# Optimization experiments

Hardware: AMD Instinct MI355X
Metric: run time of the kernel (lower is better)

## Reference

```python
import jax, jax.numpy as jnp
import numpy as np

B, S, D, H, DFF, L = 4, 1024, 512, 8, 2048, 4
HD = D // H


def _make_masks(key):
    k1, k2, k3 = jax.random.split(key, 3)
    node = jax.random.randint(k1, (B, S), 0, 128)            # entity-row id per token
    table = node % 4                                          # table id consistent per node
    col = jax.random.randint(k2, (B, S), 0, 32)               # column-name id
    f2p = jax.random.randint(k3, (B, S, 8), 0, 128)           # fk->pk neighbor node ids
    f2p = f2p.at[:, :, 0].set(node)                           # include self so diag is valid
    active = jnp.ones((B, S, S), dtype=bool)                  # no padding
    same_node = node[:, :, None] == node[:, None, :]
    kv_in_f2p = (node[:, None, :, None] == f2p[:, :, None, :]).any(-1)
    q_in_p2f = (node[:, :, None, None] == f2p[:, None, :, :]).any(-1)
    same_col_table = (col[:, :, None] == col[:, None, :]) & (table[:, :, None] == table[:, None, :])
    col_mask = same_col_table & active
    feat_mask = (same_node | kv_in_f2p) & active
    nbr_mask = q_in_p2f & active
    return col_mask, feat_mask, nbr_mask, active


def setup_inputs() -> dict:
    key = jax.random.key(0)
    ks = jax.random.split(key, 8)
    x = jax.random.normal(ks[0], (B, S, D), dtype=jnp.float32)
    norm_w = jnp.ones((L, 5, D), dtype=jnp.float32)
    attn_w = jax.random.normal(ks[1], (L, 4, 4, D, D), dtype=jnp.float32) * (D ** -0.5)
    ffn_up = jax.random.normal(ks[2], (L, D, DFF), dtype=jnp.float32) * (D ** -0.5)
    ffn_gate = jax.random.normal(ks[3], (L, D, DFF), dtype=jnp.float32) * (D ** -0.5)
    ffn_down = jax.random.normal(ks[4], (L, DFF, D), dtype=jnp.float32) * (DFF ** -0.5)
    col_mask, feat_mask, nbr_mask, full_mask = _make_masks(ks[5])
    return {"x": x, "norm_w": norm_w, "attn_w": attn_w, "ffn_up": ffn_up,
            "ffn_gate": ffn_gate, "ffn_down": ffn_down, "col_mask": col_mask,
            "feat_mask": feat_mask, "nbr_mask": nbr_mask, "full_mask": full_mask}


def _rmsnorm(x, w):
    eps = jnp.finfo(x.dtype).eps
    return x * jax.lax.rsqrt(jnp.mean(x * x, axis=-1, keepdims=True) + eps) * w


def _masked_attn(x, mask, w):
    # w: [4, D, D] = (wq, wk, wv, wo); mask: [b, s, s] bool
    b, s, d = x.shape
    def split_heads(y):
        return y.reshape(b, s, H, HD).transpose(0, 2, 1, 3)  # b h s hd
    q = split_heads(x @ w[0])
    k = split_heads(x @ w[1])
    v = split_heads(x @ w[2])
    scores = jnp.einsum('bhqd,bhkd->bhqk', q, k) * (HD ** -0.5)
    m = mask[:, None, :, :]
    neg = jnp.where(m, scores, -1e30)
    mx = jnp.max(neg, axis=-1, keepdims=True)
    e = jnp.exp(neg - mx) * m
    den = jnp.maximum(e.sum(axis=-1, keepdims=True), 1e-20)  # fully-masked rows -> 0 output
    out = jnp.einsum('bhqk,bhkd->bhqd', e / den, v)
    out = out.transpose(0, 2, 1, 3).reshape(b, s, d)
    return out @ w[3]


def _ffn(x, up, gate, down):
    return (jax.nn.silu(x @ gate) * (x @ up)) @ down


def reference(x, norm_w, attn_w, ffn_up, ffn_gate, ffn_down, col_mask, feat_mask, nbr_mask, full_mask):
    masks = (col_mask, feat_mask, nbr_mask, full_mask)

    def block(h, p):
        nw, aw, up, gate, down = p
        for i in range(4):
            h = h + _masked_attn(_rmsnorm(h, nw[i]), masks[i], aw[i])
        h = h + _ffn(_rmsnorm(h, nw[4]), up, gate, down)
        return h, None

    out, _ = jax.lax.scan(block, x, (norm_w, attn_w, ffn_up, ffn_gate, ffn_down))
    return out
```

## Files before the change

### kernel.cpp

```cpp
#include <hip/hip_runtime.h>
#include <cstdint>
#include <cstddef>

#define B_   4
#define S_   1024
#define D_   512
#define H_   8
#define HD_  64
#define DFF_ 2048
#define L_   4
#define M_   (B_ * S_)

typedef unsigned long long ull;
typedef __attribute__((ext_vector_type(8))) short bf16x8;
typedef __attribute__((ext_vector_type(4))) float f32x4;

__device__ __forceinline__ ushort f2bf(float f) {
  uint32_t u = __float_as_uint(f);
  u += 0x7fffu + ((u >> 16) & 1u);
  return (ushort)(u >> 16);
}
__device__ __forceinline__ float bf2f(ushort b) {
  return __uint_as_float(((uint32_t)b) << 16);
}
__device__ __forceinline__ void g2lds16(const void* g, void* l) {
  __builtin_amdgcn_global_load_lds((const __attribute__((address_space(1))) unsigned int*)g,
                                   (__attribute__((address_space(3))) unsigned int*)l, 16, 0, 0);
}

__global__ __launch_bounds__(256) void wtrans_kernel(const float* __restrict__ in,
                                                     ushort* __restrict__ out,
                                                     int R, int C, size_t ims, size_t oms) {
  __shared__ float tile[32][33];
  const int tx = threadIdx.x & 31, ty = threadIdx.x >> 5;
  const int c0 = blockIdx.x * 32, r0 = blockIdx.y * 32;
  const float* ip = in + (size_t)blockIdx.z * ims;
  ushort* op = out + (size_t)blockIdx.z * oms;
  #pragma unroll
  for (int i = 0; i < 4; ++i) tile[ty + 8 * i][tx] = ip[(size_t)(r0 + ty + 8 * i) * C + c0 + tx];
  __syncthreads();
  #pragma unroll
  for (int i = 0; i < 4; ++i) op[(size_t)(c0 + ty + 8 * i) * R + r0 + tx] = f2bf(tile[tx][ty + 8 * i]);
}

__global__ __launch_bounds__(256) void maskpack_kernel(const void* m0, const void* m1,
                                                       const void* m2, const void* m3,
                                                       ull* __restrict__ out,
                                                       const unsigned char* __restrict__ probe) {
  const int mi = blockIdx.y;
  const void* mp = (mi == 0) ? m0 : (mi == 1) ? m1 : (mi == 2) ? m2 : m3;
  const int wid = blockIdx.x * 256 + threadIdx.x;
  const int row = wid >> 4, ch = wid & 15;
  ull bits = 0;
  if (probe[1] == 0) {
    const int4* p = (const int4*)mp + (((size_t)row * 1024 + ch * 64) >> 2);
    #pragma unroll
    for (int k = 0; k < 16; ++k) {
      const int4 v = p[k];
      bits |= (ull)(v.x != 0) << (k * 4 + 0);
      bits |= (ull)(v.y != 0) << (k * 4 + 1);
      bits |= (ull)(v.z != 0) << (k * 4 + 2);
      bits |= (ull)(v.w != 0) << (k * 4 + 3);
    }
  } else {
    const uint4* p = (const uint4*)((const unsigned char*)mp + (size_t)row * 1024 + ch * 64);
    #pragma unroll
    for (int k = 0; k < 4; ++k) {
      const uint4 v = p[k];
      const uint32_t w4[4] = {v.x, v.y, v.z, v.w};
      #pragma unroll
      for (int w = 0; w < 4; ++w)
        #pragma unroll
        for (int bb = 0; bb < 4; ++bb)
          bits |= (ull)(((w4[w] >> (8 * bb)) & 0xffu) ? 1 : 0) << (k * 16 + w * 4 + bb);
    }
  }
  out[(size_t)mi * 65536 + wid] = bits;
}

__global__ __launch_bounds__(256) void rmsnorm_kernel(const float* __restrict__ x,
                                                      const float* __restrict__ w,
                                                      ushort* __restrict__ y) {
  const int row = blockIdx.x;
  const float2 v = ((const float2*)(x + (size_t)row * D_))[threadIdx.x];
  float ss = v.x * v.x + v.y * v.y;
  #pragma unroll
  for (int off = 32; off > 0; off >>= 1) ss += __shfl_down(ss, off);
  __shared__ float sred[4];
  if ((threadIdx.x & 63) == 0) sred[threadIdx.x >> 6] = ss;
  __syncthreads();
  const float tot = sred[0] + sred[1] + sred[2] + sred[3];
  const float scale = rsqrtf(tot * (1.0f / (float)D_) + 1.1920929e-07f);
  const float2 wv = ((const float2*)w)[threadIdx.x];
  const uint32_t o = (uint32_t)f2bf(v.x * scale * wv.x) | ((uint32_t)f2bf(v.y * scale * wv.y) << 16);
  ((uint32_t*)(y + (size_t)row * D_))[threadIdx.x] = o;
}

__global__ __launch_bounds__(256) void gemm_bf16_kernel(const ushort* __restrict__ A, int lda,
                                                        const ushort* __restrict__ Wt, int K,
                                                        void* __restrict__ Cout, int ldc,
                                                        int mode) {
  __shared__ __align__(16) uint8_t lds[32768];
  const int t = threadIdx.x, l = t & 63, wv = t >> 6;
  const int m0 = blockIdx.y * 128, n0 = blockIdx.x * 128;
  const int wrow = (wv >> 1) * 64, wcol = (wv & 1) * 64;

  f32x4 acc[4][4] = {};
  const int nk = K / 64;
  for (int kt = 0; kt < nk; ++kt) {
    __syncthreads();
    {
      const int k0 = kt * 64;
      #pragma unroll
      for (int i = 0; i < 4; ++i) {
        const int row = wv * 32 + i * 8 + (l >> 3);
        const int g = (l & 7) ^ (row & 7);
        g2lds16(A + (size_t)(m0 + row) * lda + k0 + g * 8, &lds[(wv * 32 + i * 8) * 128]);
        g2lds16(Wt + (size_t)(n0 + row) * K + k0 + g * 8, &lds[16384 + (wv * 32 + i * 8) * 128]);
      }
    }
    __syncthreads();
    const uint8_t* Ab = &lds[0];
    const uint8_t* Bb = &lds[16384];
    #pragma unroll
    for (int ks = 0; ks < 2; ++ks) {
      bf16x8 af[4], bfr[4];
      #pragma unroll
      for (int fm = 0; fm < 4; ++fm) {
        const int row = wrow + fm * 16 + (l & 15);
        const int chunk = ((l >> 4) + ks * 4) ^ (row & 7);
        af[fm] = *(const bf16x8*)&Ab[row * 128 + chunk * 16];
      }
      #pragma unroll
      for (int fn = 0; fn < 4; ++fn) {
        const int row = wcol + fn * 16 + (l & 15);
        const int chunk = ((l >> 4) + ks * 4) ^ (row & 7);
        bfr[fn] = *(const bf16x8*)&Bb[row * 128 + chunk * 16];
      }
      #pragma unroll
      for (int fm = 0; fm < 4; ++fm)
        #pragma unroll
        for (int fn = 0; fn < 4; ++fn)
          acc[fm][fn] = __builtin_amdgcn_mfma_f32_16x16x32_bf16(af[fm], bfr[fn], acc[fm][fn], 0, 0, 0);
    }
  }
  #pragma unroll
  for (int fm = 0; fm < 4; ++fm)
    #pragma unroll
    for (int fn = 0; fn < 4; ++fn)
      #pragma unroll
      for (int r = 0; r < 4; ++r) {
        const int row = m0 + wrow + fm * 16 + (l >> 4) * 4 + r;
        const int col = n0 + wcol + fn * 16 + (l & 15);
        const float v = acc[fm][fn][r];
        if (mode == 0) {
          ((ushort*)Cout)[(size_t)row * ldc + col] = f2bf(v);
        } else {
          float* p = (float*)Cout + (size_t)row * ldc + col;
          *p += v;
        }
      }
}

__global__ __launch_bounds__(256) void vtrans_kernel(const ushort* __restrict__ qkv,
                                                     ushort* __restrict__ vt) {
  __shared__ __align__(16) ushort tile[64][80];
  const int st = blockIdx.x, bh = blockIdx.y;
  const int b = bh >> 3, h = bh & 7;
  const int t = threadIdx.x;
  #pragma unroll
  for (int i = 0; i < 2; ++i) {
    const int id = t + 256 * i;
    const int s = id >> 3, c8 = id & 7;
    const ushort* src = qkv + (size_t)(b * S_ + st * 64 + s) * 1536 + 1024 + h * 64 + c8 * 8;
    *(bf16x8*)&tile[s][c8 * 8] = *(const bf16x8*)src;
  }
  __syncthreads();
  #pragma unroll
  for (int i = 0; i < 2; ++i) {
    const int id = t + 256 * i;
    const int d = id >> 3, s8 = id & 7;
    bf16x8 v8;
    #pragma unroll
    for (int j = 0; j < 8; ++j) v8[j] = (short)tile[s8 * 8 + j][d];
    *(bf16x8*)(vt + (size_t)(bh * 64 + d) * S_ + st * 64 + s8 * 8) = v8;
  }
}

__global__ __launch_bounds__(256) void flash_mfma_kernel(const ushort* __restrict__ qkv,
                                                         const ushort* __restrict__ vt,
                                                         const ull* __restrict__ pm,
                                                         ushort* __restrict__ att) {
  __shared__ __align__(16) uint8_t Kt[64 * 128];
  __shared__ __align__(16) uint8_t Vl[64 * 128];
  __shared__ __align__(16) uint8_t Pl[64 * 128];
  __shared__ ull Ml[64];
  const int qt = blockIdx.x, h = blockIdx.y, b = blockIdx.z;
  const int t = threadIdx.x, l = t & 63, wv = t >> 6;

  bf16x8 qf[2];
  {
    const ushort* qrow =
        qkv + (size_t)(b * S_ + qt * 64 + wv * 16 + (l & 15)) * 1536 + h * HD_ + (l >> 4) * 8;
    qf[0] = *(const bf16x8*)qrow;
    qf[1] = *(const bf16x8*)(qrow + 32);
  }
  f32x4 oacc[4] = {};
  float mrow[4] = {-1e30f, -1e30f, -1e30f, -1e30f};
  float lrow[4] = {};

  for (int kt2 = 0; kt2 < S_ / 64; ++kt2) {
    __syncthreads();
    #pragma unroll
    for (int i = 0; i < 2; ++i) {
      const int row = i * 32 + wv * 8 + (l >> 3);
      const int g = (l & 7) ^ (row & 7);
      g2lds16(qkv + (size_t)(b * S_ + kt2 * 64 + row) * 1536 + 512 + h * HD_ + g * 8,
              &Kt[(i * 32 + wv * 8) * 128]);
      g2lds16(vt + (size_t)((b * H_ + h) * HD_ + row) * S_ + kt2 * 64 + g * 8,
              &Vl[(i * 32 + wv * 8) * 128]);
    }
    if (t < 64) Ml[t] = pm[(size_t)(b * S_ + qt * 64 + t) * 16 + kt2];
    __syncthreads();

    f32x4 sacc[4] = {};
    bf16x8 kf[4][2];
    #pragma unroll
    for (int fn = 0; fn < 4; ++fn)
      #pragma unroll
      for (int ks = 0; ks < 2; ++ks) {
        const int row = fn * 16 + (l & 15);
        const int chunk = ((l >> 4) + ks * 4) ^ (row & 7);
        kf[fn][ks] = *(const bf16x8*)&Kt[row * 128 + chunk * 16];
      }
    __builtin_amdgcn_s_setprio(1);
    #pragma unroll
    for (int fn = 0; fn < 4; ++fn)
      #pragma unroll
      for (int ks = 0; ks < 2; ++ks)
        sacc[fn] = __builtin_amdgcn_mfma_f32_16x16x32_bf16(qf[ks], kf[fn][ks], sacc[fn], 0, 0, 0);
    __builtin_amdgcn_s_setprio(0);

    float p[4][4];
    float corr[4];
    #pragma unroll
    for (int r = 0; r < 4; ++r) {
      const ull mw = Ml[wv * 16 + (l >> 4) * 4 + r];
      float s[4];
      int bit[4];
      float mx = -1e30f;
      #pragma unroll
      for (int fn = 0; fn < 4; ++fn) {
        bit[fn] = (int)((mw >> ((l & 15) + fn * 16)) & 1ull);
        const float sv = bit[fn] ? sacc[fn][r] * 0.125f : -1e30f;
        s[fn] = sv;
        mx = fmaxf(mx, sv);
      }
      mx = fmaxf(mx, __shfl_xor(mx, 1));
      mx = fmaxf(mx, __shfl_xor(mx, 2));
      mx = fmaxf(mx, __shfl_xor(mx, 4));
      mx = fmaxf(mx, __shfl_xor(mx, 8));
      const float mn = fmaxf(mrow[r], mx);
      corr[r] = __expf(mrow[r] - mn);
      mrow[r] = mn;
      float rs = 0.0f;
      #pragma unroll
      for (int fn = 0; fn < 4; ++fn) {
        const float e = bit[fn] ? __expf(s[fn] - mn) : 0.0f;
        p[fn][r] = e;
        rs += e;
      }
      rs += __shfl_xor(rs, 1);
      rs += __shfl_xor(rs, 2);
      rs += __shfl_xor(rs, 4);
      rs += __shfl_xor(rs, 8);
      lrow[r] = lrow[r] * corr[r] + rs;
    }
    #pragma unroll
    for (int fd = 0; fd < 4; ++fd)
      #pragma unroll
      for (int r = 0; r < 4; ++r) oacc[fd][r] *= corr[r];

    #pragma unroll
    for (int fn = 0; fn < 4; ++fn)
      #pragma unroll
      for (int r = 0; r < 4; ++r) {
        const int ql = (l >> 4) * 4 + r;
        const int kv = (l & 15) + fn * 16;
        *(ushort*)&Pl[(wv * 16 + ql) * 128 + (((kv >> 3) ^ (ql & 7)) * 16) + (kv & 7) * 2] =
            f2bf(p[fn][r]);
      }
    __syncthreads();

    bf16x8 pa[2];
    #pragma unroll
    for (int ks = 0; ks < 2; ++ks) {
      const int row = wv * 16 + (l & 15);
      const int chunk = ((l >> 4) + ks * 4) ^ ((l & 15) & 7);
      pa[ks] = *(const bf16x8*)&Pl[row * 128 + chunk * 16];
    }
    bf16x8 vf[4][2];
    #pragma unroll
    for (int fd = 0; fd < 4; ++fd)
      #pragma unroll
      for (int ks = 0; ks < 2; ++ks) {
        const int row = fd * 16 + (l & 15);
        const int chunk = ((l >> 4) + ks * 4) ^ (row & 7);
        vf[fd][ks] = *(const bf16x8*)&Vl[row * 128 + chunk * 16];
      }
    __builtin_amdgcn_s_setprio(1);
    #pragma unroll
    for (int fd = 0; fd < 4; ++fd)
      #pragma unroll
      for (int ks = 0; ks < 2; ++ks)
        oacc[fd] = __builtin_amdgcn_mfma_f32_16x16x32_bf16(pa[ks], vf[fd][ks], oacc[fd], 0, 0, 0);
    __builtin_amdgcn_s_setprio(0);
  }

  #pragma unroll
  for (int r = 0; r < 4; ++r) {
    const float inv = 1.0f / fmaxf(lrow[r], 1e-20f);
    #pragma unroll
    for (int fd = 0; fd < 4; ++fd) {
      att[(size_t)(b * S_ + qt * 64 + wv * 16 + (l >> 4) * 4 + r) * D_ + h * HD_ + (l & 15) +
          fd * 16] = f2bf(oacc[fd][r] * inv);
    }
  }
}

__global__ __launch_bounds__(256) void silu_kernel(ushort* __restrict__ gu) {
  const int idx = blockIdx.x * 256 + threadIdx.x;
  const int row = idx >> 8, c8 = idx & 255;
  ushort* gp = gu + (size_t)row * 4096 + c8 * 8;
  const ushort* up = gp + 2048;
  bf16x8 g8 = *(const bf16x8*)gp;
  const bf16x8 u8 = *(const bf16x8*)up;
  #pragma unroll
  for (int j = 0; j < 8; ++j) {
    const float g = bf2f((ushort)g8[j]);
    const float u = bf2f((ushort)u8[j]);
    g8[j] = (short)f2bf(g / (1.0f + __expf(-g)) * u);
  }
  *(bf16x8*)gp = g8;
}

extern "C" void kernel_launch(void* const* d_in, const int* in_sizes, int n_in,
                              void* d_out, int out_size, void* d_ws, size_t ws_size,
                              hipStream_t stream) {
  const float* x        = (const float*)d_in[0];
  const float* norm_w   = (const float*)d_in[1];
  const float* attn_w   = (const float*)d_in[2];
  const float* ffn_up   = (const float*)d_in[3];
  const float* ffn_gate = (const float*)d_in[4];
  const float* ffn_down = (const float*)d_in[5];

  float* h = (float*)d_out;
  ushort* wt_attn = (ushort*)d_ws;
  ushort* wt_gu   = wt_attn + (size_t)16 * 512 * 512;
  ushort* wt_down = wt_gu + (size_t)4096 * 512;
  ull*    pmask   = (ull*)(wt_down + (size_t)512 * 2048);
  ushort* y       = (ushort*)(pmask + 4 * 65536);
  ushort* qkvbuf  = y + (size_t)M_ * 512;
  ushort* vt      = qkvbuf + (size_t)M_ * 1536;
  ushort* att     = vt + (size_t)M_ * 512;
  ushort* gu      = qkvbuf;

  hipMemcpyAsync(h, x, sizeof(float) * (size_t)M_ * D_, hipMemcpyDeviceToDevice, stream);

  const dim3 blk(256);
  maskpack_kernel<<<dim3(256, 4), blk, 0, stream>>>(d_in[6], d_in[7], d_in[8], d_in[9], pmask,
                                                    (const unsigned char*)d_in[9]);

  for (int l = 0; l < L_; ++l) {
    wtrans_kernel<<<dim3(16, 16, 16), blk, 0, stream>>>(
        attn_w + (size_t)l * 16 * 512 * 512, wt_attn, 512, 512, 512 * 512, 512 * 512);
    wtrans_kernel<<<dim3(64, 16, 1), blk, 0, stream>>>(
        ffn_gate + (size_t)l * 512 * 2048, wt_gu, 512, 2048, 0, 0);
    wtrans_kernel<<<dim3(64, 16, 1), blk, 0, stream>>>(
        ffn_up + (size_t)l * 512 * 2048, wt_gu + (size_t)2048 * 512, 512, 2048, 0, 0);
    wtrans_kernel<<<dim3(16, 64, 1), blk, 0, stream>>>(
        ffn_down + (size_t)l * 2048 * 512, wt_down, 2048, 512, 0, 0);

    for (int i = 0; i < 4; ++i) {
      rmsnorm_kernel<<<M_, blk, 0, stream>>>(h, norm_w + (size_t)(l * 5 + i) * D_, y);
      gemm_bf16_kernel<<<dim3(12, 32), blk, 0, stream>>>(
          y, 512, wt_attn + (size_t)i * 4 * 512 * 512, 512, qkvbuf, 1536, 0);
      vtrans_kernel<<<dim3(16, 32), blk, 0, stream>>>(qkvbuf, vt);
      flash_mfma_kernel<<<dim3(16, 8, 4), blk, 0, stream>>>(qkvbuf, vt, pmask + (size_t)i * 65536,
                                                            att);
      gemm_bf16_kernel<<<dim3(4, 32), blk, 0, stream>>>(
          att, 512, wt_attn + (size_t)i * 4 * 512 * 512 + (size_t)1536 * 512, 512, h, 512, 1);
    }
    rmsnorm_kernel<<<M_, blk, 0, stream>>>(h, norm_w + (size_t)(l * 5 + 4) * D_, y);
    gemm_bf16_kernel<<<dim3(32, 32), blk, 0, stream>>>(y, 512, wt_gu, 512, gu, 4096, 0);
    silu_kernel<<<dim3(M_ * 2048 / 8 / 256), blk, 0, stream>>>(gu);
    gemm_bf16_kernel<<<dim3(4, 32), blk, 0, stream>>>(gu, 4096, wt_down, 2048, h, 512, 1);
  }
}
```

Measured before the change: 2.051 ms.

## Fuse V-transpose and SiLU into GEMM epilogues, widen flash KV tile, retile GEMMs

The QKV GEMM epilogue now writes V directly in transposed layout, which removes the separate vtrans kernel. A new dual-accumulator gate/up GEMM applies SiLU·up in its epilogue, which drops the silu kernel and the round trip through the 4096-wide buffer. The flash kernel now processes 128 keys per iteration to halve the number of barrier-separated iterations, at the cost of more LDS and registers. The output and down projections use a 64-row M tile to double the block count, and rmsnorm handles one row per wavefront with float4 loads and no LDS reduction. The V-transpose epilogue writes scattered 2-byte stores, and the gate/up kernel holds two 4x4 accumulator sets, so register pressure rises.

```diff
diff --git a/kernel.cpp b/kernel.cpp
--- a/kernel.cpp
+++ b/kernel.cpp
@@ -81,52 +81,68 @@
 __global__ __launch_bounds__(256) void rmsnorm_kernel(const float* __restrict__ x,
                                                       const float* __restrict__ w,
                                                       ushort* __restrict__ y) {
-  const int row = blockIdx.x;
-  const float2 v = ((const float2*)(x + (size_t)row * D_))[threadIdx.x];
-  float ss = v.x * v.x + v.y * v.y;
-  #pragma unroll
-  for (int off = 32; off > 0; off >>= 1) ss += __shfl_down(ss, off);
-  __shared__ float sred[4];
-  if ((threadIdx.x & 63) == 0) sred[threadIdx.x >> 6] = ss;
-  __syncthreads();
-  const float tot = sred[0] + sred[1] + sred[2] + sred[3];
-  const float scale = rsqrtf(tot * (1.0f / (float)D_) + 1.1920929e-07f);
-  const float2 wv = ((const float2*)w)[threadIdx.x];
-  const uint32_t o = (uint32_t)f2bf(v.x * scale * wv.x) | ((uint32_t)f2bf(v.y * scale * wv.y) << 16);
-  ((uint32_t*)(y + (size_t)row * D_))[threadIdx.x] = o;
-}
-
+  const int row = blockIdx.x * 4 + (threadIdx.x >> 6);
+  const int l = threadIdx.x & 63;
+  const float4* xr = (const float4*)(x + (size_t)row * D_);
+  const float4 v0 = xr[l * 2], v1 = xr[l * 2 + 1];
+  float ss = v0.x * v0.x + v0.y * v0.y + v0.z * v0.z + v0.w * v0.w +
+             v1.x * v1.x + v1.y * v1.y + v1.z * v1.z + v1.w * v1.w;
+  #pragma unroll
+  for (int off = 32; off > 0; off >>= 1) ss += __shfl_xor(ss, off);
+  const float scale = rsqrtf(ss * (1.0f / (float)D_) + 1.1920929e-07f);
+  const float4* wr = (const float4*)w;
+  const float4 w0 = wr[l * 2], w1 = wr[l * 2 + 1];
+  bf16x8 o;
+  o[0] = (short)f2bf(v0.x * scale * w0.x);
+  o[1] = (short)f2bf(v0.y * scale * w0.y);
+  o[2] = (short)f2bf(v0.z * scale * w0.z);
+  o[3] = (short)f2bf(v0.w * scale * w0.w);
+  o[4] = (short)f2bf(v1.x * scale * w1.x);
+  o[5] = (short)f2bf(v1.y * scale * w1.y);
+  o[6] = (short)f2bf(v1.z * scale * w1.z);
+  o[7] = (short)f2bf(v1.w * scale * w1.w);
+  *(bf16x8*)(y + (size_t)row * D_ + l * 8) = o;
+}
+
+template <int BM>
 __global__ __launch_bounds__(256) void gemm_bf16_kernel(const ushort* __restrict__ A, int lda,
                                                         const ushort* __restrict__ Wt, int K,
                                                         void* __restrict__ Cout, int ldc,
-                                                        int mode) {
-  __shared__ __align__(16) uint8_t lds[32768];
+                                                        int mode, ushort* __restrict__ vt) {
+  constexpr int MR = BM / 32;
+  __shared__ __align__(16) uint8_t lds[BM * 128 + 16384];
   const int t = threadIdx.x, l = t & 63, wv = t >> 6;
-  const int m0 = blockIdx.y * 128, n0 = blockIdx.x * 128;
-  const int wrow = (wv >> 1) * 64, wcol = (wv & 1) * 64;
-
-  f32x4 acc[4][4] = {};
+  const int m0 = blockIdx.y * BM, n0 = blockIdx.x * 128;
+  const int wrow = (wv >> 1) * (BM / 2), wcol = (wv & 1) * 64;
+
+  f32x4 acc[MR][4] = {};
   const int nk = K / 64;
   for (int kt = 0; kt < nk; ++kt) {
     __syncthreads();
     {
       const int k0 = kt * 64;
+      #pragma unroll
+      for (int i = 0; i < BM / 32; ++i) {
+        const int row = wv * (BM / 4) + i * 8 + (l >> 3);
+        const int g = (l & 7) ^ (row & 7);
+        g2lds16(A + (size_t)(m0 + row) * lda + k0 + g * 8, &lds[(wv * (BM / 4) + i * 8) * 128]);
+      }
       #pragma unroll
       for (int i = 0; i < 4; ++i) {
         const int row = wv * 32 + i * 8 + (l >> 3);
         const int g = (l & 7) ^ (row & 7);
-        g2lds16(A + (size_t)(m0 + row) * lda + k0 + g * 8, &lds[(wv * 32 + i * 8) * 128]);
-        g2lds16(Wt + (size_t)(n0 + row) * K + k0 + g * 8, &lds[16384 + (wv * 32 + i * 8) * 128]);
+        g2lds16(Wt + (size_t)(n0 + row) * K + k0 + g * 8,
+                &lds[BM * 128 + (wv * 32 + i * 8) * 128]);
       }
     }
     __syncthreads();
     const uint8_t* Ab = &lds[0];
-    const uint8_t* Bb = &lds[16384];
+    const uint8_t* Bb = &lds[BM * 128];
     #pragma unroll
     for (int ks = 0; ks < 2; ++ks) {
-      bf16x8 af[4], bfr[4];
-      #pragma unroll
-      for (int fm = 0; fm < 4; ++fm) {
+      bf16x8 af[MR], bfr[4];
+      #pragma unroll
+      for (int fm = 0; fm < MR; ++fm) {
         const int row = wrow + fm * 16 + (l & 15);
         const int chunk = ((l >> 4) + ks * 4) ^ (row & 7);
         af[fm] = *(const bf16x8*)&Ab[row * 128 + chunk * 16];
@@ -138,14 +154,14 @@
         bfr[fn] = *(const bf16x8*)&Bb[row * 128 + chunk * 16];
       }
       #pragma unroll
-      for (int fm = 0; fm < 4; ++fm)
+      for (int fm = 0; fm < MR; ++fm)
         #pragma unroll
         for (int fn = 0; fn < 4; ++fn)
           acc[fm][fn] = __builtin_amdgcn_mfma_f32_16x16x32_bf16(af[fm], bfr[fn], acc[fm][fn], 0, 0, 0);
     }
   }
   #pragma unroll
-  for (int fm = 0; fm < 4; ++fm)
+  for (int fm = 0; fm < MR; ++fm)
     #pragma unroll
     for (int fn = 0; fn < 4; ++fn)
       #pragma unroll
@@ -153,55 +169,107 @@
         const int row = m0 + wrow + fm * 16 + (l >> 4) * 4 + r;
         const int col = n0 + wcol + fn * 16 + (l & 15);
         const float v = acc[fm][fn][r];
-        if (mode == 0) {
-          ((ushort*)Cout)[(size_t)row * ldc + col] = f2bf(v);
-        } else {
+        if (mode == 1) {
           float* p = (float*)Cout + (size_t)row * ldc + col;
           *p += v;
+        } else {
+          if (col < 1024) {
+            ((ushort*)Cout)[(size_t)row * ldc + col] = f2bf(v);
+          } else {
+            const int hh = (col - 1024) >> 6, dd = (col - 1024) & 63;
+            const int bb = row >> 10, ss = row & 1023;
+            vt[((size_t)(bb * 8 + hh) * 64 + dd) * 1024 + ss] = f2bf(v);
+          }
         }
       }
 }
 
-__global__ __launch_bounds__(256) void vtrans_kernel(const ushort* __restrict__ qkv,
-                                                     ushort* __restrict__ vt) {
-  __shared__ __align__(16) ushort tile[64][80];
-  const int st = blockIdx.x, bh = blockIdx.y;
-  const int b = bh >> 3, h = bh & 7;
-  const int t = threadIdx.x;
-  #pragma unroll
-  for (int i = 0; i < 2; ++i) {
-    const int id = t + 256 * i;
-    const int s = id >> 3, c8 = id & 7;
-    const ushort* src = qkv + (size_t)(b * S_ + st * 64 + s) * 1536 + 1024 + h * 64 + c8 * 8;
-    *(bf16x8*)&tile[s][c8 * 8] = *(const bf16x8*)src;
-  }
-  __syncthreads();
-  #pragma unroll
-  for (int i = 0; i < 2; ++i) {
-    const int id = t + 256 * i;
-    const int d = id >> 3, s8 = id & 7;
-    bf16x8 v8;
-    #pragma unroll
-    for (int j = 0; j < 8; ++j) v8[j] = (short)tile[s8 * 8 + j][d];
-    *(bf16x8*)(vt + (size_t)(bh * 64 + d) * S_ + st * 64 + s8 * 8) = v8;
-  }
+__global__ __launch_bounds__(256) void gemm_gateup_kernel(const ushort* __restrict__ A,
+                                                          const ushort* __restrict__ Wg,
+                                                          const ushort* __restrict__ Wu,
+                                                          ushort* __restrict__ sg) {
+  __shared__ __align__(16) uint8_t lds[49152];
+  const int t = threadIdx.x, l = t & 63, wv = t >> 6;
+  const int m0 = blockIdx.y * 128, n0 = blockIdx.x * 128;
+  const int wrow = (wv >> 1) * 64, wcol = (wv & 1) * 64;
+
+  f32x4 accg[4][4] = {}, accu[4][4] = {};
+  for (int kt = 0; kt < 8; ++kt) {
+    __syncthreads();
+    {
+      const int k0 = kt * 64;
+      #pragma unroll
+      for (int i = 0; i < 4; ++i) {
+        const int row = wv * 32 + i * 8 + (l >> 3);
+        const int g = (l & 7) ^ (row & 7);
+        g2lds16(A + (size_t)(m0 + row) * 512 + k0 + g * 8, &lds[(wv * 32 + i * 8) * 128]);
+        g2lds16(Wg + (size_t)(n0 + row) * 512 + k0 + g * 8, &lds[16384 + (wv * 32 + i * 8) * 128]);
+        g2lds16(Wu + (size_t)(n0 + row) * 512 + k0 + g * 8, &lds[32768 + (wv * 32 + i * 8) * 128]);
+      }
+    }
+    __syncthreads();
+    #pragma unroll
+    for (int ks = 0; ks < 2; ++ks) {
+      bf16x8 af[4], bf[4];
+      #pragma unroll
+      for (int fm = 0; fm < 4; ++fm) {
+        const int row = wrow + fm * 16 + (l & 15);
+        const int chunk = ((l >> 4) + ks * 4) ^ (row & 7);
+        af[fm] = *(const bf16x8*)&lds[row * 128 + chunk * 16];
+      }
+      #pragma unroll
+      for (int fn = 0; fn < 4; ++fn) {
+        const int row = wcol + fn * 16 + (l & 15);
+        const int chunk = ((l >> 4) + ks * 4) ^ (row & 7);
+        bf[fn] = *(const bf16x8*)&lds[16384 + row * 128 + chunk * 16];
+      }
+      #pragma unroll
+      for (int fm = 0; fm < 4; ++fm)
+        #pragma unroll
+        for (int fn = 0; fn < 4; ++fn)
+          accg[fm][fn] = __builtin_amdgcn_mfma_f32_16x16x32_bf16(af[fm], bf[fn], accg[fm][fn], 0, 0, 0);
+      #pragma unroll
+      for (int fn = 0; fn < 4; ++fn) {
+        const int row = wcol + fn * 16 + (l & 15);
+        const int chunk = ((l >> 4) + ks * 4) ^ (row & 7);
+        bf[fn] = *(const bf16x8*)&lds[32768 + row * 128 + chunk * 16];
+      }
+      #pragma unroll
+      for (int fm = 0; fm < 4; ++fm)
+        #pragma unroll
+        for (int fn = 0; fn < 4; ++fn)
+          accu[fm][fn] = __builtin_amdgcn_mfma_f32_16x16x32_bf16(af[fm], bf[fn], accu[fm][fn], 0, 0, 0);
+    }
+  }
+  #pragma unroll
+  for (int fm = 0; fm < 4; ++fm)
+    #pragma unroll
+    for (int fn = 0; fn < 4; ++fn)
+      #pragma unroll
+      for (int r = 0; r < 4; ++r) {
+        const int row = m0 + wrow + fm * 16 + (l >> 4) * 4 + r;
+        const int col = n0 + wcol + fn * 16 + (l & 15);
+        const float g = accg[fm][fn][r];
+        const float u = accu[fm][fn][r];
+        sg[(size_t)row * 2048 + col] = f2bf(g / (1.0f + __expf(-g)) * u);
+      }
 }
 
 __global__ __launch_bounds__(256) void flash_mfma_kernel(const ushort* __restrict__ qkv,
                                                          const ushort* __restrict__ vt,
                                                          const ull* __restrict__ pm,
                                                          ushort* __restrict__ att) {
-  __shared__ __align__(16) uint8_t Kt[64 * 128];
-  __shared__ __align__(16) uint8_t Vl[64 * 128];
-  __shared__ __align__(16) uint8_t Pl[64 * 128];
-  __shared__ ull Ml[64];
+  __shared__ __align__(16) uint8_t Kt[128 * 128];
+  __shared__ __align__(16) uint8_t Vl[64 * 256];
+  __shared__ __align__(16) uint8_t Pl[64 * 256];
+  __shared__ ull Ml[128];
   const int qt = blockIdx.x, h = blockIdx.y, b = blockIdx.z;
   const int t = threadIdx.x, l = t & 63, wv = t >> 6;
 
   bf16x8 qf[2];
   {
     const ushort* qrow =
-        qkv + (size_t)(b * S_ + qt * 64 + wv * 16 + (l & 15)) * 1536 + h * HD_ + (l >> 4) * 8;
+        qkv + (size_t)(b * S_ + qt * 64 + wv * 16 + (l & 15)) * 1024 + h * HD_ + (l >> 4) * 8;
     qf[0] = *(const bf16x8*)qrow;
     qf[1] = *(const bf16x8*)(qrow + 32);
   }
@@ -209,49 +277,51 @@
   float mrow[4] = {-1e30f, -1e30f, -1e30f, -1e30f};
   float lrow[4] = {};
 
-  for (int kt2 = 0; kt2 < S_ / 64; ++kt2) {
-    __syncthreads();
-    #pragma unroll
-    for (int i = 0; i < 2; ++i) {
-      const int row = i * 32 + wv * 8 + (l >> 3);
+  for (int kt2 = 0; kt2 < S_ / 128; ++kt2) {
+    __syncthreads();
+    #pragma unroll
+    for (int i = 0; i < 4; ++i) {
+      const int row = wv * 32 + i * 8 + (l >> 3);
       const int g = (l & 7) ^ (row & 7);
-      g2lds16(qkv + (size_t)(b * S_ + kt2 * 64 + row) * 1536 + 512 + h * HD_ + g * 8,
-              &Kt[(i * 32 + wv * 8) * 128]);
-      g2lds16(vt + (size_t)((b * H_ + h) * HD_ + row) * S_ + kt2 * 64 + g * 8,
-              &Vl[(i * 32 + wv * 8) * 128]);
-    }
-    if (t < 64) Ml[t] = pm[(size_t)(b * S_ + qt * 64 + t) * 16 + kt2];
-    __syncthreads();
-
-    f32x4 sacc[4] = {};
-    bf16x8 kf[4][2];
-    #pragma unroll
-    for (int fn = 0; fn < 4; ++fn)
+      g2lds16(qkv + (size_t)(b * S_ + kt2 * 128 + row) * 1024 + 512 + h * HD_ + g * 8,
+              &Kt[(wv * 32 + i * 8) * 128]);
+    }
+    #pragma unroll
+    for (int i = 0; i < 4; ++i) {
+      const int d = wv * 16 + i * 4 + (l >> 4);
+      const int c = (l & 15) ^ (d & 7);
+      g2lds16(vt + ((size_t)(b * 8 + h) * 64 + d) * 1024 + kt2 * 128 + c * 8,
+              &Vl[(wv * 16 + i * 4) * 256]);
+    }
+    if (t < 128) Ml[t] = pm[(size_t)(b * S_ + qt * 64 + (t >> 1)) * 16 + kt2 * 2 + (t & 1)];
+    __syncthreads();
+
+    f32x4 sacc[8] = {};
+    __builtin_amdgcn_s_setprio(1);
+    #pragma unroll
+    for (int fn = 0; fn < 8; ++fn) {
+      const int row = fn * 16 + (l & 15);
       #pragma unroll
       for (int ks = 0; ks < 2; ++ks) {
-        const int row = fn * 16 + (l & 15);
-        const int chunk = ((l >> 4) + ks * 4) ^ (row & 7);
-        kf[fn][ks] = *(const bf16x8*)&Kt[row * 128 + chunk * 16];
-      }
-    __builtin_amdgcn_s_setprio(1);
-    #pragma unroll
-    for (int fn = 0; fn < 4; ++fn)
-      #pragma unroll
-      for (int ks = 0; ks < 2; ++ks)
-        sacc[fn] = __builtin_amdgcn_mfma_f32_16x16x32_bf16(qf[ks], kf[fn][ks], sacc[fn], 0, 0, 0);
+        const int chunk = ((l >> 4) + ks * 4) ^ (row & 7);
+        const bf16x8 kf = *(const bf16x8*)&Kt[row * 128 + chunk * 16];
+        sacc[fn] = __builtin_amdgcn_mfma_f32_16x16x32_bf16(qf[ks], kf, sacc[fn], 0, 0, 0);
+      }
+    }
     __builtin_amdgcn_s_setprio(0);
 
-    float p[4][4];
+    float p[8][4];
     float corr[4];
     #pragma unroll
     for (int r = 0; r < 4; ++r) {
-      const ull mw = Ml[wv * 16 + (l >> 4) * 4 + r];
-      float s[4];
-      int bit[4];
+      const int qloc = wv * 16 + (l >> 4) * 4 + r;
+      const ull mw0 = Ml[2 * qloc], mw1 = Ml[2 * qloc + 1];
+      float s[8];
+      int bit[8];
       float mx = -1e30f;
       #pragma unroll
-      for (int fn = 0; fn < 4; ++fn) {
-        bit[fn] = (int)((mw >> ((l & 15) + fn * 16)) & 1ull);
+      for (int fn = 0; fn < 8; ++fn) {
+        bit[fn] = (int)(((fn < 4 ? mw0 : mw1) >> ((l & 15) + (fn & 3) * 16)) & 1ull);
         const float sv = bit[fn] ? sacc[fn][r] * 0.125f : -1e30f;
         s[fn] = sv;
         mx = fmaxf(mx, sv);
@@ -265,7 +335,7 @@
       mrow[r] = mn;
       float rs = 0.0f;
       #pragma unroll
-      for (int fn = 0; fn < 4; ++fn) {
+      for (int fn = 0; fn < 8; ++fn) {
         const float e = bit[fn] ? __expf(s[fn] - mn) : 0.0f;
         p[fn][r] = e;
         rs += e;
@@ -282,38 +352,34 @@
       for (int r = 0; r < 4; ++r) oacc[fd][r] *= corr[r];
 
     #pragma unroll
-    for (int fn = 0; fn < 4; ++fn)
+    for (int fn = 0; fn < 8; ++fn)
       #pragma unroll
       for (int r = 0; r < 4; ++r) {
         const int ql = (l >> 4) * 4 + r;
         const int kv = (l & 15) + fn * 16;
-        *(ushort*)&Pl[(wv * 16 + ql) * 128 + (((kv >> 3) ^ (ql & 7)) * 16) + (kv & 7) * 2] =
+        *(ushort*)&Pl[(wv * 16 + ql) * 256 + (((kv >> 3) ^ (ql & 7)) * 16) + (kv & 7) * 2] =
             f2bf(p[fn][r]);
       }
     __syncthreads();
 
-    bf16x8 pa[2];
-    #pragma unroll
-    for (int ks = 0; ks < 2; ++ks) {
+    bf16x8 pa[4];
+    #pragma unroll
+    for (int ks = 0; ks < 4; ++ks) {
       const int row = wv * 16 + (l & 15);
       const int chunk = ((l >> 4) + ks * 4) ^ ((l & 15) & 7);
-      pa[ks] = *(const bf16x8*)&Pl[row * 128 + chunk * 16];
-    }
-    bf16x8 vf[4][2];
-    #pragma unroll
-    for (int fd = 0; fd < 4; ++fd)
-      #pragma unroll
-      for (int ks = 0; ks < 2; ++ks) {
-        const int row = fd * 16 + (l & 15);
-        const int chunk = ((l >> 4) + ks * 4) ^ (row & 7);
-        vf[fd][ks] = *(const bf16x8*)&Vl[row * 128 + chunk * 16];
-      }
+      pa[ks] = *(const bf16x8*)&Pl[row * 256 + chunk * 16];
+    }
     __builtin_amdgcn_s_setprio(1);
     #pragma unroll
-    for (int fd = 0; fd < 4; ++fd)
-      #pragma unroll
-      for (int ks = 0; ks < 2; ++ks)
-        oacc[fd] = __builtin_amdgcn_mfma_f32_16x16x32_bf16(pa[ks], vf[fd][ks], oacc[fd], 0, 0, 0);
+    for (int fd = 0; fd < 4; ++fd) {
+      const int rowd = fd * 16 + (l & 15);
+      #pragma unroll
+      for (int ks = 0; ks < 4; ++ks) {
+        const int chunk = ((l >> 4) + ks * 4) ^ (rowd & 7);
+        const bf16x8 vf = *(const bf16x8*)&Vl[rowd * 256 + chunk * 16];
+        oacc[fd] = __builtin_amdgcn_mfma_f32_16x16x32_bf16(pa[ks], vf, oacc[fd], 0, 0, 0);
+      }
+    }
     __builtin_amdgcn_s_setprio(0);
   }
 
@@ -326,22 +392,6 @@
           fd * 16] = f2bf(oacc[fd][r] * inv);
     }
   }
-}
-
-__global__ __launch_bounds__(256) void silu_kernel(ushort* __restrict__ gu) {
-  const int idx = blockIdx.x * 256 + threadIdx.x;
-  const int row = idx >> 8, c8 = idx & 255;
-  ushort* gp = gu + (size_t)row * 4096 + c8 * 8;
-  const ushort* up = gp + 2048;
-  bf16x8 g8 = *(const bf16x8*)gp;
-  const bf16x8 u8 = *(const bf16x8*)up;
-  #pragma unroll
-  for (int j = 0; j < 8; ++j) {
-    const float g = bf2f((ushort)g8[j]);
-    const float u = bf2f((ushort)u8[j]);
-    g8[j] = (short)f2bf(g / (1.0f + __expf(-g)) * u);
-  }
-  *(bf16x8*)gp = g8;
 }
 
 extern "C" void kernel_launch(void* const* d_in, const int* in_sizes, int n_in,
@@ -357,13 +407,13 @@
   float* h = (float*)d_out;
   ushort* wt_attn = (ushort*)d_ws;
   ushort* wt_gu   = wt_attn + (size_t)16 * 512 * 512;
-  ushort* wt_down = wt_gu + (size_t)4096 * 512;
+  ushort* wt_down = wt_gu + (size_t)2 * 2048 * 512;
   ull*    pmask   = (ull*)(wt_down + (size_t)512 * 2048);
   ushort* y       = (ushort*)(pmask + 4 * 65536);
   ushort* qkvbuf  = y + (size_t)M_ * 512;
-  ushort* vt      = qkvbuf + (size_t)M_ * 1536;
+  ushort* vt      = qkvbuf + (size_t)M_ * 1024;
   ushort* att     = vt + (size_t)M_ * 512;
-  ushort* gu      = qkvbuf;
+  ushort* sg      = att + (size_t)M_ * 512;
 
   hipMemcpyAsync(h, x, sizeof(float) * (size_t)M_ * D_, hipMemcpyDeviceToDevice, stream);
 
@@ -382,18 +432,18 @@
         ffn_down + (size_t)l * 2048 * 512, wt_down, 2048, 512, 0, 0);
 
     for (int i = 0; i < 4; ++i) {
-      rmsnorm_kernel<<<M_, blk, 0, stream>>>(h, norm_w + (size_t)(l * 5 + i) * D_, y);
-      gemm_bf16_kernel<<<dim3(12, 32), blk, 0, stream>>>(
-          y, 512, wt_attn + (size_t)i * 4 * 512 * 512, 512, qkvbuf, 1536, 0);
-      vtrans_kernel<<<dim3(16, 32), blk, 0, stream>>>(qkvbuf, vt);
+      rmsnorm_kernel<<<M_ / 4, blk, 0, stream>>>(h, norm_w + (size_t)(l * 5 + i) * D_, y);
+      gemm_bf16_kernel<128><<<dim3(12, 32), blk, 0, stream>>>(
+          y, 512, wt_attn + (size_t)i * 4 * 512 * 512, 512, qkvbuf, 1024, 2, vt);
       flash_mfma_kernel<<<dim3(16, 8, 4), blk, 0, stream>>>(qkvbuf, vt, pmask + (size_t)i * 65536,
                                                             att);
-      gemm_bf16_kernel<<<dim3(4, 32), blk, 0, stream>>>(
-          att, 512, wt_attn + (size_t)i * 4 * 512 * 512 + (size_t)1536 * 512, 512, h, 512, 1);
-    }
-    rmsnorm_kernel<<<M_, blk, 0, stream>>>(h, norm_w + (size_t)(l * 5 + 4) * D_, y);
-    gemm_bf16_kernel<<<dim3(32, 32), blk, 0, stream>>>(y, 512, wt_gu, 512, gu, 4096, 0);
-    silu_kernel<<<dim3(M_ * 2048 / 8 / 256), blk, 0, stream>>>(gu);
-    gemm_bf16_kernel<<<dim3(4, 32), blk, 0, stream>>>(gu, 4096, wt_down, 2048, h, 512, 1);
-  }
-}
+      gemm_bf16_kernel<64><<<dim3(4, 64), blk, 0, stream>>>(
+          att, 512, wt_attn + (size_t)i * 4 * 512 * 512 + (size_t)1536 * 512, 512, h, 512, 1,
+          nullptr);
+    }
+    rmsnorm_kernel<<<M_ / 4, blk, 0, stream>>>(h, norm_w + (size_t)(l * 5 + 4) * D_, y);
+    gemm_gateup_kernel<<<dim3(16, 32), blk, 0, stream>>>(y, wt_gu, wt_gu + (size_t)2048 * 512, sg);
+    gemm_bf16_kernel<64><<<dim3(4, 64), blk, 0, stream>>>(sg, 2048, wt_down, 2048, h, 512, 1,
+                                                          nullptr);
+  }
+}
```

Result: faster. 1.767 ms (-13.9%).
